# Performance work log

Measured on AMD Instinct MI355X. Metric: run time of the kernel, lower is better.

Reference implementation:

```python
import jax, jax.numpy as jnp
import numpy as np

K = 3  # knnLoss default k


def _knn_loss(source_pc, target_pc, k=K):
    """Faithful translation of knnLoss.forward.

    For each batch: drop exact-zero (0,0,0) points from both clouds
    (emulated via masking for static shapes), find the k nearest *target*
    points for every *source* point (query=source, ref=target), take the
    mean Euclidean distance, then average over batch.
    """

    def per_batch(src, tgt):  # src, tgt: [N, 3]
        src_valid = jnp.any(src != 0.0, axis=-1)  # [Ns] move_zero_point mask
        tgt_valid = jnp.any(tgt != 0.0, axis=-1)  # [Nt]
        s2 = jnp.sum(src * src, axis=-1)          # [Ns]
        t2 = jnp.sum(tgt * tgt, axis=-1)          # [Nt]
        # squared pairwise distances, [Ns, Nt]
        d2 = s2[:, None] + t2[None, :] - 2.0 * (src @ tgt.T)
        d2 = jnp.maximum(d2, 0.0)
        # invalid (zero) target points can never be a neighbor
        d2 = jnp.where(tgt_valid[None, :], d2, jnp.inf)
        neg_top, _ = jax.lax.top_k(-d2, k)        # k smallest squared dists
        dist = jnp.sqrt(-neg_top)                 # [Ns, k] euclidean, like KNN_CUDA
        # mean over valid source points x k neighbors
        num = jnp.sum(jnp.where(src_valid[:, None], dist, 0.0))
        den = jnp.sum(src_valid).astype(dist.dtype) * k
        return num / den

    return jnp.mean(jax.vmap(per_batch)(source_pc, target_pc))


def setup_inputs() -> dict:
    key = jax.random.key(0)
    k1, k2 = jax.random.split(key)
    B, N = 4, 8192
    source_pc = jax.random.normal(k1, (B, N, 3), dtype=jnp.float32)
    target_pc = jax.random.normal(k2, (B, N, 3), dtype=jnp.float32)
    return {"source_pc": source_pc, "target_pc": target_pc}


def reference(source_pc, target_pc):
    return _knn_loss(source_pc, target_pc)
```

## Files before the change

### kernel.cpp

```cpp
#include <hip/hip_runtime.h>
#include <math.h>

#define BATCH 4
#define NPTS 8192
#define TILE 512
#define NTILES 16
#define SLOTS 4
#define ROUNDS 4
#define SRC_PER_BLOCK 64
#define NBLOCKS (BATCH * NPTS / SRC_PER_BLOCK)
#define NOCT 64
#define OCTF 36
#define SLOTF (NOCT * OCTF)

typedef __attribute__((ext_vector_type(2))) float f2;

__device__ __forceinline__ float min3f(float a, float b, float c) {
    float d;
    asm("v_min3_f32 %0, %1, %2, %3" : "=v"(d) : "v"(a), "v"(b), "v"(c));
    return d;
}

__device__ __forceinline__ void insert3(float d, float& a0, float& a1, float& a2) {
    float h = fmaxf(a1, d);
    float m = __builtin_amdgcn_fmed3f(a0, a1, d);
    a2 = fminf(a2, h);
    a1 = m;
    a0 = fminf(a0, d);
}

__device__ __forceinline__ void merge33(float a0, float a1, float a2,
                                        float& b0, float& b1, float& b2) {
    float s0 = fminf(a0, b0);
    float h  = fmaxf(a0, b0);
    float m  = fminf(a1, b1);
    float mm = fminf(a2, b2);
    b1 = fminf(h, m);
    b2 = __builtin_amdgcn_fmed3f(h, m, mm);
    b0 = s0;
}

__device__ __forceinline__ void octet_insert(const float4* ob, f2 nx, f2 ny, f2 nz,
                                             float& c0, float& c1, float& c2) {
    float4 X0 = ob[0], X1 = ob[1], Y0 = ob[2], Y1 = ob[3];
    float4 Z0 = ob[4], Z1 = ob[5], W0 = ob[6], W1 = ob[7];
    f2 pa = __builtin_elementwise_fma((f2){Z0.x, Z0.y}, nz, (f2){W0.x, W0.y});
    pa = __builtin_elementwise_fma((f2){Y0.x, Y0.y}, ny, pa);
    pa = __builtin_elementwise_fma((f2){X0.x, X0.y}, nx, pa);
    f2 pb = __builtin_elementwise_fma((f2){Z0.z, Z0.w}, nz, (f2){W0.z, W0.w});
    pb = __builtin_elementwise_fma((f2){Y0.z, Y0.w}, ny, pb);
    pb = __builtin_elementwise_fma((f2){X0.z, X0.w}, nx, pb);
    f2 pc = __builtin_elementwise_fma((f2){Z1.x, Z1.y}, nz, (f2){W1.x, W1.y});
    pc = __builtin_elementwise_fma((f2){Y1.x, Y1.y}, ny, pc);
    pc = __builtin_elementwise_fma((f2){X1.x, X1.y}, nx, pc);
    f2 pd = __builtin_elementwise_fma((f2){Z1.z, Z1.w}, nz, (f2){W1.z, W1.w});
    pd = __builtin_elementwise_fma((f2){Y1.z, Y1.w}, ny, pd);
    pd = __builtin_elementwise_fma((f2){X1.z, X1.w}, nx, pd);
    insert3(pa.x, c0, c1, c2);
    insert3(pa.y, c0, c1, c2);
    insert3(pb.x, c0, c1, c2);
    insert3(pb.y, c0, c1, c2);
    insert3(pc.x, c0, c1, c2);
    insert3(pc.y, c0, c1, c2);
    insert3(pd.x, c0, c1, c2);
    insert3(pd.y, c0, c1, c2);
}

__global__ __launch_bounds__(256) void knn_fused(const float* __restrict__ src,
                                                 const float* __restrict__ tgt,
                                                 float* __restrict__ acc,
                                                 float* __restrict__ cnt,
                                                 unsigned* __restrict__ ticket,
                                                 float* __restrict__ out) {
    __shared__ float tsf[SLOTS * SLOTF];
    const int tid = threadIdx.x;
    const int lane = tid & 63, wave = tid >> 6;
    const int bid = blockIdx.x;
    const int gid = bid * SRC_PER_BLOCK + lane;
    const int b = bid >> 7;

    const float* sp = src + (size_t)gid * 3;
    float ax = sp[0], ay = sp[1], az = sp[2];
    f2 nx = (f2){-2.f * ax, -2.f * ax};
    f2 ny = (f2){-2.f * ay, -2.f * ay};
    f2 nz = (f2){-2.f * az, -2.f * az};

    float e0 = 3e38f, e1 = 3e38f, e2 = 3e38f;

    for (int r = 0; r < ROUNDS; ++r) {
        __syncthreads();
        #pragma unroll
        for (int j = 0; j < 4; ++j) {
            int p = j * 256 + tid;
            const float* tb = tgt + ((size_t)b * NPTS + r * (SLOTS * TILE) + 2 * p) * 3;
            float x0 = tb[0], y0 = tb[1], z0 = tb[2];
            float x1 = tb[3], y1 = tb[4], z1 = tb[5];
            float w0 = x0 * x0 + y0 * y0 + z0 * z0;
            float w1 = x1 * x1 + y1 * y1 + z1 * z1;
            if (!(x0 != 0.f || y0 != 0.f || z0 != 0.f)) w0 = 3.0e38f;
            if (!(x1 != 0.f || y1 != 0.f || z1 != 0.f)) w1 = 3.0e38f;
            int sl = p >> 8;
            int o = (p >> 2) & 63;
            int k = (2 * p) & 7;
            int base = sl * SLOTF + o * OCTF + ((k >> 2) << 2) + (k & 3);
            *(float2*)(tsf + base)      = make_float2(x0, x1);
            *(float2*)(tsf + base + 8)  = make_float2(y0, y1);
            *(float2*)(tsf + base + 16) = make_float2(z0, z1);
            *(float2*)(tsf + base + 24) = make_float2(w0, w1);
        }
        __syncthreads();

        const float4* tsv = (const float4*)(tsf + wave * SLOTF);
        float q0 = 3e38f, q1 = 3e38f, q2 = 3e38f;
        #pragma unroll 2
        for (int o = 0; o < NOCT; ++o) {
            float4 X0 = tsv[9 * o + 0], X1 = tsv[9 * o + 1];
            float4 Y0 = tsv[9 * o + 2], Y1 = tsv[9 * o + 3];
            float4 Z0 = tsv[9 * o + 4], Z1 = tsv[9 * o + 5];
            float4 W0 = tsv[9 * o + 6], W1 = tsv[9 * o + 7];
            f2 pa = __builtin_elementwise_fma((f2){Z0.x, Z0.y}, nz, (f2){W0.x, W0.y});
            pa = __builtin_elementwise_fma((f2){Y0.x, Y0.y}, ny, pa);
            pa = __builtin_elementwise_fma((f2){X0.x, X0.y}, nx, pa);
            f2 pb = __builtin_elementwise_fma((f2){Z0.z, Z0.w}, nz, (f2){W0.z, W0.w});
            pb = __builtin_elementwise_fma((f2){Y0.z, Y0.w}, ny, pb);
            pb = __builtin_elementwise_fma((f2){X0.z, X0.w}, nx, pb);
            f2 pc = __builtin_elementwise_fma((f2){Z1.x, Z1.y}, nz, (f2){W1.x, W1.y});
            pc = __builtin_elementwise_fma((f2){Y1.x, Y1.y}, ny, pc);
            pc = __builtin_elementwise_fma((f2){X1.x, X1.y}, nx, pc);
            f2 pd = __builtin_elementwise_fma((f2){Z1.z, Z1.w}, nz, (f2){W1.z, W1.w});
            pd = __builtin_elementwise_fma((f2){Y1.z, Y1.w}, ny, pd);
            pd = __builtin_elementwise_fma((f2){X1.z, X1.w}, nx, pd);
            float m1 = min3f(pa.x, pa.y, pb.x);
            float m2 = min3f(pb.y, pc.x, pc.y);
            float m3 = min3f(pd.x, pd.y, m1);
            float m4 = fminf(m2, m3);
            unsigned u = (__float_as_uint(m4) & 0xFFFFFFC0u) | (unsigned)o;
            insert3(__uint_as_float(u), q0, q1, q2);
        }
        octet_insert(tsv + 9 * (int)(__float_as_uint(q0) & 63u), nx, ny, nz, e0, e1, e2);
        octet_insert(tsv + 9 * (int)(__float_as_uint(q1) & 63u), nx, ny, nz, e0, e1, e2);
        octet_insert(tsv + 9 * (int)(__float_as_uint(q2) & 63u), nx, ny, nz, e0, e1, e2);
    }

    __syncthreads();
    tsf[wave * 64 + lane]       = e0;
    tsf[256 + wave * 64 + lane] = e1;
    tsf[512 + wave * 64 + lane] = e2;
    __syncthreads();

    if (tid < 64) {
        float a0 = tsf[lane], a1 = tsf[256 + lane], a2 = tsf[512 + lane];
        #pragma unroll
        for (int g = 1; g < 4; ++g)
            merge33(tsf[g * 64 + lane], tsf[256 + g * 64 + lane],
                    tsf[512 + g * 64 + lane], a0, a1, a2);

        bool valid = (ax != 0.f) || (ay != 0.f) || (az != 0.f);
        float qq = ax * ax + ay * ay + az * az;
        float s = valid ? (sqrtf(fmaxf(a0 + qq, 0.f)) + sqrtf(fmaxf(a1 + qq, 0.f)) +
                           sqrtf(fmaxf(a2 + qq, 0.f)))
                        : 0.f;
        float c = valid ? 1.f : 0.f;

        for (int off = 32; off >= 1; off >>= 1) {
            s += __shfl_down(s, off);
            c += __shfl_down(c, off);
        }
        if (lane == 0) {
            atomicAdd(&acc[b], s);
            atomicAdd(&cnt[b], c);
            __threadfence();
            unsigned t = atomicAdd(ticket, 1u);
            if (t == (unsigned)(NBLOCKS - 1)) {
                float loss = 0.f;
                #pragma unroll
                for (int bb = 0; bb < BATCH; ++bb) {
                    float as = atomicAdd(&acc[bb], 0.f);
                    float ac = atomicAdd(&cnt[bb], 0.f);
                    loss += as / (ac * 3.0f);
                }
                out[0] = loss * (1.0f / BATCH);
            }
        }
    }
}

extern "C" void kernel_launch(void* const* d_in, const int* in_sizes, int n_in,
                              void* d_out, int out_size, void* d_ws, size_t ws_size,
                              hipStream_t stream) {
    const float* src = (const float*)d_in[0];
    const float* tgt = (const float*)d_in[1];
    float* out = (float*)d_out;

    float* acc = (float*)d_ws;
    float* cnt = acc + 4;
    unsigned* ticket = (unsigned*)((char*)d_ws + 32);

    hipMemsetAsync(d_ws, 0, 64, stream);
    knn_fused<<<dim3(NBLOCKS), 256, 0, stream>>>(src, tgt, acc, cnt, ticket, out);
}
```

Measured before the change: 112.4 us.

## Split each wave's target scan across two half-waves and halve sources per block

Each block now handles 32 source points instead of 64. Each wave's two 32-lane halves scan separate halves of the 64 octets of staged targets, and the per-source results from eight chains are merged at the end. This doubles the number of blocks and shortens each thread's serial octet loop, aiming for better CU fill and latency hiding. Target tiles are now loaded with float2 vector loads, and a launch-bounds occupancy hint is added. In exchange, target staging into LDS and global target reads double in total across the grid, and the final merge is longer.

```diff
diff --git a/kernel.cpp b/kernel.cpp
--- a/kernel.cpp
+++ b/kernel.cpp
@@ -4,10 +4,9 @@
 #define BATCH 4
 #define NPTS 8192
 #define TILE 512
-#define NTILES 16
 #define SLOTS 4
 #define ROUNDS 4
-#define SRC_PER_BLOCK 64
+#define SRC_PER_BLOCK 32
 #define NBLOCKS (BATCH * NPTS / SRC_PER_BLOCK)
 #define NOCT 64
 #define OCTF 36
@@ -66,18 +65,20 @@
     insert3(pd.y, c0, c1, c2);
 }
 
-__global__ __launch_bounds__(256) void knn_fused(const float* __restrict__ src,
-                                                 const float* __restrict__ tgt,
-                                                 float* __restrict__ acc,
-                                                 float* __restrict__ cnt,
-                                                 unsigned* __restrict__ ticket,
-                                                 float* __restrict__ out) {
+__global__ __launch_bounds__(256, 4) void knn_fused(const float* __restrict__ src,
+                                                    const float* __restrict__ tgt,
+                                                    float* __restrict__ acc,
+                                                    float* __restrict__ cnt,
+                                                    unsigned* __restrict__ ticket,
+                                                    float* __restrict__ out) {
     __shared__ float tsf[SLOTS * SLOTF];
     const int tid = threadIdx.x;
     const int lane = tid & 63, wave = tid >> 6;
+    const int slane = lane & 31;
+    const int half = lane >> 5;
     const int bid = blockIdx.x;
-    const int gid = bid * SRC_PER_BLOCK + lane;
-    const int b = bid >> 7;
+    const int gid = bid * SRC_PER_BLOCK + slane;
+    const int b = bid >> 8;
 
     const float* sp = src + (size_t)gid * 3;
     float ax = sp[0], ay = sp[1], az = sp[2];
@@ -92,9 +93,11 @@
         #pragma unroll
         for (int j = 0; j < 4; ++j) {
             int p = j * 256 + tid;
-            const float* tb = tgt + ((size_t)b * NPTS + r * (SLOTS * TILE) + 2 * p) * 3;
-            float x0 = tb[0], y0 = tb[1], z0 = tb[2];
-            float x1 = tb[3], y1 = tb[4], z1 = tb[5];
+            const float2* tb2 = (const float2*)(tgt +
+                ((size_t)b * NPTS + r * (SLOTS * TILE) + 2 * p) * 3);
+            float2 A = tb2[0], Bv = tb2[1], C = tb2[2];
+            float x0 = A.x, y0 = A.y, z0 = Bv.x;
+            float x1 = Bv.y, y1 = C.x, z1 = C.y;
             float w0 = x0 * x0 + y0 * y0 + z0 * z0;
             float w1 = x1 * x1 + y1 * y1 + z1 * z1;
             if (!(x0 != 0.f || y0 != 0.f || z0 != 0.f)) w0 = 3.0e38f;
@@ -110,14 +113,14 @@
         }
         __syncthreads();
 
-        const float4* tsv = (const float4*)(tsf + wave * SLOTF);
+        const float4* tsv = (const float4*)(tsf + wave * SLOTF) + 9 * 32 * half;
         float q0 = 3e38f, q1 = 3e38f, q2 = 3e38f;
         #pragma unroll 2
-        for (int o = 0; o < NOCT; ++o) {
-            float4 X0 = tsv[9 * o + 0], X1 = tsv[9 * o + 1];
-            float4 Y0 = tsv[9 * o + 2], Y1 = tsv[9 * o + 3];
-            float4 Z0 = tsv[9 * o + 4], Z1 = tsv[9 * o + 5];
-            float4 W0 = tsv[9 * o + 6], W1 = tsv[9 * o + 7];
+        for (int j = 0; j < 32; ++j) {
+            float4 X0 = tsv[9 * j + 0], X1 = tsv[9 * j + 1];
+            float4 Y0 = tsv[9 * j + 2], Y1 = tsv[9 * j + 3];
+            float4 Z0 = tsv[9 * j + 4], Z1 = tsv[9 * j + 5];
+            float4 W0 = tsv[9 * j + 6], W1 = tsv[9 * j + 7];
             f2 pa = __builtin_elementwise_fma((f2){Z0.x, Z0.y}, nz, (f2){W0.x, W0.y});
             pa = __builtin_elementwise_fma((f2){Y0.x, Y0.y}, ny, pa);
             pa = __builtin_elementwise_fma((f2){X0.x, X0.y}, nx, pa);
@@ -134,26 +137,27 @@
             float m2 = min3f(pb.y, pc.x, pc.y);
             float m3 = min3f(pd.x, pd.y, m1);
             float m4 = fminf(m2, m3);
-            unsigned u = (__float_as_uint(m4) & 0xFFFFFFC0u) | (unsigned)o;
+            unsigned u = (__float_as_uint(m4) & 0xFFFFFFE0u) | (unsigned)j;
             insert3(__uint_as_float(u), q0, q1, q2);
         }
-        octet_insert(tsv + 9 * (int)(__float_as_uint(q0) & 63u), nx, ny, nz, e0, e1, e2);
-        octet_insert(tsv + 9 * (int)(__float_as_uint(q1) & 63u), nx, ny, nz, e0, e1, e2);
-        octet_insert(tsv + 9 * (int)(__float_as_uint(q2) & 63u), nx, ny, nz, e0, e1, e2);
+        octet_insert(tsv + 9 * (int)(__float_as_uint(q0) & 31u), nx, ny, nz, e0, e1, e2);
+        octet_insert(tsv + 9 * (int)(__float_as_uint(q1) & 31u), nx, ny, nz, e0, e1, e2);
+        octet_insert(tsv + 9 * (int)(__float_as_uint(q2) & 31u), nx, ny, nz, e0, e1, e2);
     }
 
     __syncthreads();
-    tsf[wave * 64 + lane]       = e0;
-    tsf[256 + wave * 64 + lane] = e1;
-    tsf[512 + wave * 64 + lane] = e2;
+    int chain = (wave * 2 + half) * 32 + slane;
+    tsf[chain]       = e0;
+    tsf[256 + chain] = e1;
+    tsf[512 + chain] = e2;
     __syncthreads();
 
-    if (tid < 64) {
-        float a0 = tsf[lane], a1 = tsf[256 + lane], a2 = tsf[512 + lane];
+    if (tid < 32) {
+        float a0 = tsf[tid], a1 = tsf[256 + tid], a2 = tsf[512 + tid];
         #pragma unroll
-        for (int g = 1; g < 4; ++g)
-            merge33(tsf[g * 64 + lane], tsf[256 + g * 64 + lane],
-                    tsf[512 + g * 64 + lane], a0, a1, a2);
+        for (int g = 1; g < 8; ++g)
+            merge33(tsf[g * 32 + tid], tsf[256 + g * 32 + tid],
+                    tsf[512 + g * 32 + tid], a0, a1, a2);
 
         bool valid = (ax != 0.f) || (ay != 0.f) || (az != 0.f);
         float qq = ax * ax + ay * ay + az * az;
@@ -162,11 +166,11 @@
                         : 0.f;
         float c = valid ? 1.f : 0.f;
 
-        for (int off = 32; off >= 1; off >>= 1) {
+        for (int off = 16; off >= 1; off >>= 1) {
             s += __shfl_down(s, off);
             c += __shfl_down(c, off);
         }
-        if (lane == 0) {
+        if (tid == 0) {
             atomicAdd(&acc[b], s);
             atomicAdd(&cnt[b], c);
             __threadfence();
```

Result: slower. 120.3 us (+7.0%).
